# Performance work log

Hardware: AMD Instinct MI355X
Metric: run time of the kernel (lower is better)

Reference implementation:

```python
import jax, jax.numpy as jnp
import numpy as np
import math

NUM_PAGES = 256   # total KV pool pages
PAGE_SIZE = 16    # tokens per page
N_USED = 128      # pages in this sequence -> kv_len = 2048
H = 32            # num_heads
D = 128           # head_dim
LQ = 2048         # query length (== kv_len, causal prefill)


def setup_inputs() -> dict:
    key = jax.random.key(0)
    k_q, k_k, k_v, k_ks, k_vs = jax.random.split(key, 5)
    q = jax.random.normal(k_q, (1, H, LQ, D), dtype=jnp.float32)
    K_pages = jax.random.randint(k_k, (NUM_PAGES, PAGE_SIZE, H, D), -128, 128, dtype=jnp.int8)
    V_pages = jax.random.randint(k_v, (NUM_PAGES, PAGE_SIZE, H, D), -128, 128, dtype=jnp.int8)
    K_scale = jax.random.uniform(k_ks, (NUM_PAGES, 1, H, 1), dtype=jnp.float16, minval=0.001, maxval=0.02)
    V_scale = jax.random.uniform(k_vs, (NUM_PAGES, 1, H, 1), dtype=jnp.float16, minval=0.001, maxval=0.02)
    pages = jnp.arange(N_USED, dtype=jnp.int32)  # page table for this sequence
    return {"q": q, "K_pages": K_pages, "V_pages": V_pages,
            "K_scale": K_scale, "V_scale": V_scale, "pages": pages}


def _gather_dequant(pages_i8, scales, page_ids):
    # pages_i8: [P, ps, H, D] int8; scales: [P, 1, H, 1] fp16; page_ids: [n]
    x = pages_i8[page_ids].astype(jnp.float32) * scales[page_ids].astype(jnp.float32)
    n, ps, h, d = x.shape
    # cat along tokens, then [S,H,D] -> [1,H,S,D]
    return jnp.transpose(x.reshape(n * ps, h, d), (1, 0, 2))[None]


def reference(q, K_pages, V_pages, K_scale, V_scale, pages):
    K = _gather_dequant(K_pages, K_scale, pages)  # [1,H,S,D]
    V = _gather_dequant(V_pages, V_scale, pages)  # [1,H,S,D]
    lq = q.shape[2]
    s = K.shape[2]
    scale = 1.0 / math.sqrt(q.shape[-1])
    scores = jnp.einsum('bhqd,bhkd->bhqk', q, K) * scale  # [1,H,LQ,S]
    # torch is_causal: top-left aligned causal mask (j <= i)
    causal = jnp.tril(jnp.ones((lq, s), dtype=bool))
    scores = jnp.where(causal[None, None], scores, -jnp.inf)
    attn = jax.nn.softmax(scores, axis=-1)
    return jnp.einsum('bhqk,bhkd->bhqd', attn, V)
```

## Files before the change

### kernel.cpp

```cpp
#include <hip/hip_runtime.h>
#include <stdint.h>

#define NHEADS 32
#define DHEAD  128
#define LQ     2048
#define PAGE   16
#define QTILE  64
#define KVB    32
#define KPAD   136

typedef _Float16 f16x8 __attribute__((ext_vector_type(8)));
typedef float    f32x4 __attribute__((ext_vector_type(4)));

__global__ __launch_bounds__(256, 2)
void paged_attn_kernel(const float* __restrict__ q,
                       const int*   __restrict__ Kp,
                       const int*   __restrict__ Vp,
                       const float* __restrict__ Kscale,
                       const float* __restrict__ Vscale,
                       const int*   __restrict__ pages,
                       float* __restrict__ out)
{
    __shared__ _Float16 Ks[KVB][KPAD];
    __shared__ __align__(16) _Float16 Vt[DHEAD][KVB];
    __shared__ float    ksc[KVB];
    __shared__ _Float16 Ps[4][16][40];

    const int tid  = threadIdx.x;
    const int w    = tid >> 6;
    const int lane = tid & 63;
    const int g    = lane >> 4;
    const int c    = lane & 15;

    const int bx = blockIdx.x;
    const int h  = bx & (NHEADS - 1);
    const int nQT = gridDim.x >> 5;
    const int qt = nQT - 1 - (bx >> 5);
    const int q0 = qt * QTILE;

    const float qscale = 0.08838834764831845f * 1.44269504088896340736f;

    f16x8 qf[4];
    {
        const int qrow = q0 + w * 16 + c;
        const float* qp = q + ((size_t)h * LQ + qrow) * DHEAD;
        #pragma unroll
        for (int t = 0; t < 4; ++t) {
            const float* p = qp + t * 32 + g * 8;
            #pragma unroll
            for (int i = 0; i < 8; ++i)
                qf[t][i] = (_Float16)(p[i] * qscale);
        }
    }

    f32x4 o_acc[8];
    #pragma unroll
    for (int d = 0; d < 8; ++d) o_acc[d] = (f32x4){0.f, 0.f, 0.f, 0.f};
    float m_run[4], l_run[4];
    #pragma unroll
    for (int r = 0; r < 4; ++r) { m_run[r] = -1e30f; l_run[r] = 0.f; }

    const int ntiles = 2 * qt + 2;
    const int skv = tid >> 3;
    const int sa  = tid & 7;

    char* vtb = (char*)&Vt[0][0];

    auto issue = [&](int tile, int4* krD, int4* vrD, float& ksD, float& vsD) {
        const int t_glob = tile * KVB + skv;
        const int pg  = pages[t_glob >> 4];
        const int tok = t_glob & 15;
        const size_t base = (((size_t)pg * PAGE + tok) * NHEADS + h) * DHEAD + sa * 16;
        const int4* kp4 = (const int4*)(Kp + base);
        const int4* vp4 = (const int4*)(Vp + base);
        #pragma unroll
        for (int j = 0; j < 4; ++j) { krD[j] = kp4[j]; vrD[j] = vp4[j]; }
        vsD = Vscale[pg * NHEADS + h];
        if (tid < KVB) {
            const int pg2 = pages[(tile * KVB + tid) >> 4];
            ksD = Kscale[pg2 * NHEADS + h];
        }
    };

    int4 krA[4], vrA[4]; float kscA = 0.f, vsrA = 0.f;
    int4 krB[4], vrB[4]; float kscB = 0.f, vsrB = 0.f;
    issue(0, krA, vrA, kscA, vsrA);

    for (int tile = 0; tile < ntiles; ++tile) {
        const int kv0 = tile * KVB;

        {
            const int* ki = (const int*)krA;
            const int* vi = (const int*)vrA;
            f16x8 klo, khi;
            #pragma unroll
            for (int i = 0; i < 8; ++i) {
                klo[i] = (_Float16)ki[i];
                khi[i] = (_Float16)ki[8 + i];
            }
            *(f16x8*)&Ks[skv][sa * 16]     = klo;
            *(f16x8*)&Ks[skv][sa * 16 + 8] = khi;
            #pragma unroll
            for (int j = 0; j < 16; ++j) {
                const int dcol = sa * 16 + j;
                unsigned off = (unsigned)(dcol * (KVB * 2) + skv * 2);
                off ^= (unsigned)(((dcol >> 3) & 7) << 4);
                *(_Float16*)(vtb + off) = (_Float16)((float)vi[j] * vsrA);
            }
            if (tid < KVB) ksc[tid] = kscA;
        }
        __syncthreads();

        if (tile + 1 < ntiles) issue(tile + 1, krB, vrB, kscB, vsrB);

        const int q_wave_max = q0 + w * 16 + 15;
        if (kv0 <= q_wave_max) {
            f32x4 s[2];
            #pragma unroll
            for (int nt = 0; nt < 2; ++nt) {
                s[nt] = (f32x4){0.f, 0.f, 0.f, 0.f};
                #pragma unroll
                for (int t = 0; t < 4; ++t) {
                    f16x8 kf = *(const f16x8*)&Ks[nt * 16 + c][t * 32 + g * 8];
                    s[nt] = __builtin_amdgcn_mfma_f32_16x16x32_f16(qf[t], kf, s[nt], 0, 0, 0);
                }
            }
            const float ks0 = ksc[c],  ks1 = ksc[16 + c];
            const int kvg0 = kv0 + c, kvg1 = kv0 + 16 + c;
            const int qg   = q0 + w * 16 + g * 4;

            float tmax[4];
            #pragma unroll
            for (int r = 0; r < 4; ++r) {
                float s0 = s[0][r] * ks0;
                float s1 = s[1][r] * ks1;
                if (kvg0 > qg + r) s0 = -1e30f;
                if (kvg1 > qg + r) s1 = -1e30f;
                s[0][r] = s0; s[1][r] = s1;
                tmax[r] = fmaxf(s0, s1);
            }
            #pragma unroll
            for (int off = 1; off < 16; off <<= 1) {
                #pragma unroll
                for (int r = 0; r < 4; ++r)
                    tmax[r] = fmaxf(tmax[r], __shfl_xor(tmax[r], off, 64));
            }
            float alpha[4], rsum[4], p0[4], p1[4];
            #pragma unroll
            for (int r = 0; r < 4; ++r) {
                const float mn = fmaxf(m_run[r], tmax[r]);
                alpha[r] = exp2f(m_run[r] - mn);
                m_run[r] = mn;
                p0[r] = exp2f(s[0][r] - mn);
                p1[r] = exp2f(s[1][r] - mn);
                rsum[r] = p0[r] + p1[r];
            }
            #pragma unroll
            for (int off = 1; off < 16; off <<= 1) {
                #pragma unroll
                for (int r = 0; r < 4; ++r)
                    rsum[r] += __shfl_xor(rsum[r], off, 64);
            }
            #pragma unroll
            for (int r = 0; r < 4; ++r)
                l_run[r] = l_run[r] * alpha[r] + rsum[r];
            #pragma unroll
            for (int d = 0; d < 8; ++d)
                #pragma unroll
                for (int r = 0; r < 4; ++r)
                    o_acc[d][r] *= alpha[r];

            #pragma unroll
            for (int r = 0; r < 4; ++r) {
                Ps[w][g * 4 + r][c]      = (_Float16)p0[r];
                Ps[w][g * 4 + r][16 + c] = (_Float16)p1[r];
            }
            asm volatile("s_waitcnt lgkmcnt(0)" ::: "memory");
            f16x8 pf = *(const f16x8*)&Ps[w][c][g * 8];

            #pragma unroll
            for (int d = 0; d < 8; ++d) {
                const int dcol = d * 16 + c;
                unsigned off = (unsigned)(dcol * (KVB * 2) + g * 16);
                off ^= (unsigned)(((dcol >> 3) & 7) << 4);
                f16x8 vf = *(const f16x8*)(vtb + off);
                o_acc[d] = __builtin_amdgcn_mfma_f32_16x16x32_f16(pf, vf, o_acc[d], 0, 0, 0);
            }
        }
        __syncthreads();

        if (tile + 1 < ntiles) {
            #pragma unroll
            for (int j = 0; j < 4; ++j) { krA[j] = krB[j]; vrA[j] = vrB[j]; }
            kscA = kscB; vsrA = vsrB;
        }
    }

    const int qg = q0 + w * 16 + g * 4;
    float inv_l[4];
    #pragma unroll
    for (int r = 0; r < 4; ++r) inv_l[r] = 1.f / l_run[r];
    #pragma unroll
    for (int d = 0; d < 8; ++d) {
        #pragma unroll
        for (int r = 0; r < 4; ++r)
            out[((size_t)h * LQ + qg + r) * DHEAD + d * 16 + c] = o_acc[d][r] * inv_l[r];
    }
}

extern "C" void kernel_launch(void* const* d_in, const int* in_sizes, int n_in,
                              void* d_out, int out_size, void* d_ws, size_t ws_size,
                              hipStream_t stream) {
    (void)in_sizes; (void)n_in; (void)d_ws; (void)ws_size; (void)out_size;
    const float* qp = (const float*)d_in[0];
    const int*   kp = (const int*)d_in[1];
    const int*   vp = (const int*)d_in[2];
    const float* ks = (const float*)d_in[3];
    const float* vs = (const float*)d_in[4];
    const int*   pg = (const int*)d_in[5];
    float*       op = (float*)d_out;

    dim3 grid(NHEADS * (LQ / QTILE));
    dim3 block(256);
    paged_attn_kernel<<<grid, block, 0, stream>>>(qp, kp, vp, ks, vs, pg, op);
}
```

Measured before the change: 320.4 us.

## Pair complementary causal query tiles per block to balance work and reuse KV

Each block now handles two query tiles, p and NQT-1-p, for the same head, so every block does roughly the same amount of causal work. The dequantized K/V tiles staged in shared memory are shared by both query tiles, which halves KV loading and conversion per query. The grid shrinks from 1024 to 512 blocks. Each thread holds twice as many accumulators and Q fragments, which raises register pressure and may hurt occupancy under launch_bounds(256,2).

```diff
diff --git a/kernel.cpp b/kernel.cpp
--- a/kernel.cpp
+++ b/kernel.cpp
@@ -6,6 +6,7 @@
 #define LQ     2048
 #define PAGE   16
 #define QTILE  64
+#define NQT    32
 #define KVB    32
 #define KPAD   136
 
@@ -34,33 +35,34 @@
 
     const int bx = blockIdx.x;
     const int h  = bx & (NHEADS - 1);
-    const int nQT = gridDim.x >> 5;
-    const int qt = nQT - 1 - (bx >> 5);
-    const int q0 = qt * QTILE;
+    const int p  = bx >> 5;
+    const int qa = p, qb = NQT - 1 - p;
+    const int q0a = qa * QTILE, q0b = qb * QTILE;
 
     const float qscale = 0.08838834764831845f * 1.44269504088896340736f;
 
-    f16x8 qf[4];
+    f16x8 qfa[4], qfb[4];
     {
-        const int qrow = q0 + w * 16 + c;
-        const float* qp = q + ((size_t)h * LQ + qrow) * DHEAD;
+        const float* qpa = q + ((size_t)h * LQ + q0a + w * 16 + c) * DHEAD;
+        const float* qpb = q + ((size_t)h * LQ + q0b + w * 16 + c) * DHEAD;
         #pragma unroll
         for (int t = 0; t < 4; ++t) {
-            const float* p = qp + t * 32 + g * 8;
-            #pragma unroll
-            for (int i = 0; i < 8; ++i)
-                qf[t][i] = (_Float16)(p[i] * qscale);
+            #pragma unroll
+            for (int i = 0; i < 8; ++i) {
+                qfa[t][i] = (_Float16)(qpa[t * 32 + g * 8 + i] * qscale);
+                qfb[t][i] = (_Float16)(qpb[t * 32 + g * 8 + i] * qscale);
+            }
         }
     }
 
-    f32x4 o_acc[8];
-    #pragma unroll
-    for (int d = 0; d < 8; ++d) o_acc[d] = (f32x4){0.f, 0.f, 0.f, 0.f};
-    float m_run[4], l_run[4];
-    #pragma unroll
-    for (int r = 0; r < 4; ++r) { m_run[r] = -1e30f; l_run[r] = 0.f; }
-
-    const int ntiles = 2 * qt + 2;
+    f32x4 oaccA[8], oaccB[8];
+    float mA[4], lA[4], mB[4], lB[4];
+    #pragma unroll
+    for (int d = 0; d < 8; ++d) { oaccA[d] = (f32x4){0,0,0,0}; oaccB[d] = (f32x4){0,0,0,0}; }
+    #pragma unroll
+    for (int r = 0; r < 4; ++r) { mA[r] = mB[r] = -1e30f; lA[r] = lB[r] = 0.f; }
+
+    const int ntiles = 2 * qb + 2;
     const int skv = tid >> 3;
     const int sa  = tid & 7;
 
@@ -82,6 +84,79 @@
         }
     };
 
+    auto compute = [&](int kv0, const f16x8* qf, int q0t,
+                       f32x4* oacc, float* mr, float* lr) {
+        f32x4 s[2];
+        #pragma unroll
+        for (int nt = 0; nt < 2; ++nt) {
+            s[nt] = (f32x4){0,0,0,0};
+            #pragma unroll
+            for (int t = 0; t < 4; ++t) {
+                f16x8 kf = *(const f16x8*)&Ks[nt * 16 + c][t * 32 + g * 8];
+                s[nt] = __builtin_amdgcn_mfma_f32_16x16x32_f16(qf[t], kf, s[nt], 0, 0, 0);
+            }
+        }
+        const float ks0 = ksc[c],  ks1 = ksc[16 + c];
+        const int kvg0 = kv0 + c, kvg1 = kv0 + 16 + c;
+        const int qg   = q0t + w * 16 + g * 4;
+
+        float tmax[4];
+        #pragma unroll
+        for (int r = 0; r < 4; ++r) {
+            float s0 = s[0][r] * ks0;
+            float s1 = s[1][r] * ks1;
+            if (kvg0 > qg + r) s0 = -1e30f;
+            if (kvg1 > qg + r) s1 = -1e30f;
+            s[0][r] = s0; s[1][r] = s1;
+            tmax[r] = fmaxf(s0, s1);
+        }
+        #pragma unroll
+        for (int off = 1; off < 16; off <<= 1)
+            #pragma unroll
+            for (int r = 0; r < 4; ++r)
+                tmax[r] = fmaxf(tmax[r], __shfl_xor(tmax[r], off, 64));
+        float alpha[4], rsum[4], p0[4], p1[4];
+        #pragma unroll
+        for (int r = 0; r < 4; ++r) {
+            const float mn = fmaxf(mr[r], tmax[r]);
+            alpha[r] = exp2f(mr[r] - mn);
+            mr[r] = mn;
+            p0[r] = exp2f(s[0][r] - mn);
+            p1[r] = exp2f(s[1][r] - mn);
+            rsum[r] = p0[r] + p1[r];
+        }
+        #pragma unroll
+        for (int off = 1; off < 16; off <<= 1)
+            #pragma unroll
+            for (int r = 0; r < 4; ++r)
+                rsum[r] += __shfl_xor(rsum[r], off, 64);
+        #pragma unroll
+        for (int r = 0; r < 4; ++r)
+            lr[r] = lr[r] * alpha[r] + rsum[r];
+        #pragma unroll
+        for (int d = 0; d < 8; ++d)
+            #pragma unroll
+            for (int r = 0; r < 4; ++r)
+                oacc[d][r] *= alpha[r];
+
+        #pragma unroll
+        for (int r = 0; r < 4; ++r) {
+            Ps[w][g * 4 + r][c]      = (_Float16)p0[r];
+            Ps[w][g * 4 + r][16 + c] = (_Float16)p1[r];
+        }
+        asm volatile("s_waitcnt lgkmcnt(0)" ::: "memory");
+        f16x8 pf = *(const f16x8*)&Ps[w][c][g * 8];
+
+        #pragma unroll
+        for (int d = 0; d < 8; ++d) {
+            const int dcol = d * 16 + c;
+            unsigned off = (unsigned)(dcol * (KVB * 2) + g * 16);
+            off ^= (unsigned)(((dcol >> 3) & 7) << 4);
+            f16x8 vf = *(const f16x8*)(vtb + off);
+            oacc[d] = __builtin_amdgcn_mfma_f32_16x16x32_f16(pf, vf, oacc[d], 0, 0, 0);
+        }
+    };
+
     int4 krA[4], vrA[4]; float kscA = 0.f, vsrA = 0.f;
     int4 krB[4], vrB[4]; float kscB = 0.f, vsrB = 0.f;
     issue(0, krA, vrA, kscA, vsrA);
@@ -113,80 +188,11 @@
 
         if (tile + 1 < ntiles) issue(tile + 1, krB, vrB, kscB, vsrB);
 
-        const int q_wave_max = q0 + w * 16 + 15;
-        if (kv0 <= q_wave_max) {
-            f32x4 s[2];
-            #pragma unroll
-            for (int nt = 0; nt < 2; ++nt) {
-                s[nt] = (f32x4){0.f, 0.f, 0.f, 0.f};
-                #pragma unroll
-                for (int t = 0; t < 4; ++t) {
-                    f16x8 kf = *(const f16x8*)&Ks[nt * 16 + c][t * 32 + g * 8];
-                    s[nt] = __builtin_amdgcn_mfma_f32_16x16x32_f16(qf[t], kf, s[nt], 0, 0, 0);
-                }
-            }
-            const float ks0 = ksc[c],  ks1 = ksc[16 + c];
-            const int kvg0 = kv0 + c, kvg1 = kv0 + 16 + c;
-            const int qg   = q0 + w * 16 + g * 4;
-
-            float tmax[4];
-            #pragma unroll
-            for (int r = 0; r < 4; ++r) {
-                float s0 = s[0][r] * ks0;
-                float s1 = s[1][r] * ks1;
-                if (kvg0 > qg + r) s0 = -1e30f;
-                if (kvg1 > qg + r) s1 = -1e30f;
-                s[0][r] = s0; s[1][r] = s1;
-                tmax[r] = fmaxf(s0, s1);
-            }
-            #pragma unroll
-            for (int off = 1; off < 16; off <<= 1) {
-                #pragma unroll
-                for (int r = 0; r < 4; ++r)
-                    tmax[r] = fmaxf(tmax[r], __shfl_xor(tmax[r], off, 64));
-            }
-            float alpha[4], rsum[4], p0[4], p1[4];
-            #pragma unroll
-            for (int r = 0; r < 4; ++r) {
-                const float mn = fmaxf(m_run[r], tmax[r]);
-                alpha[r] = exp2f(m_run[r] - mn);
-                m_run[r] = mn;
-                p0[r] = exp2f(s[0][r] - mn);
-                p1[r] = exp2f(s[1][r] - mn);
-                rsum[r] = p0[r] + p1[r];
-            }
-            #pragma unroll
-            for (int off = 1; off < 16; off <<= 1) {
-                #pragma unroll
-                for (int r = 0; r < 4; ++r)
-                    rsum[r] += __shfl_xor(rsum[r], off, 64);
-            }
-            #pragma unroll
-            for (int r = 0; r < 4; ++r)
-                l_run[r] = l_run[r] * alpha[r] + rsum[r];
-            #pragma unroll
-            for (int d = 0; d < 8; ++d)
-                #pragma unroll
-                for (int r = 0; r < 4; ++r)
-                    o_acc[d][r] *= alpha[r];
-
-            #pragma unroll
-            for (int r = 0; r < 4; ++r) {
-                Ps[w][g * 4 + r][c]      = (_Float16)p0[r];
-                Ps[w][g * 4 + r][16 + c] = (_Float16)p1[r];
-            }
-            asm volatile("s_waitcnt lgkmcnt(0)" ::: "memory");
-            f16x8 pf = *(const f16x8*)&Ps[w][c][g * 8];
-
-            #pragma unroll
-            for (int d = 0; d < 8; ++d) {
-                const int dcol = d * 16 + c;
-                unsigned off = (unsigned)(dcol * (KVB * 2) + g * 16);
-                off ^= (unsigned)(((dcol >> 3) & 7) << 4);
-                f16x8 vf = *(const f16x8*)(vtb + off);
-                o_acc[d] = __builtin_amdgcn_mfma_f32_16x16x32_f16(pf, vf, o_acc[d], 0, 0, 0);
-            }
-        }
+        if (kv0 <= q0b + w * 16 + 15)
+            compute(kv0, qfb, q0b, oaccB, mB, lB);
+        if (kv0 <= q0a + w * 16 + 15)
+            compute(kv0, qfa, q0a, oaccA, mA, lA);
+
         __syncthreads();
 
         if (tile + 1 < ntiles) {
@@ -196,15 +202,17 @@
         }
     }
 
-    const int qg = q0 + w * 16 + g * 4;
-    float inv_l[4];
-    #pragma unroll
-    for (int r = 0; r < 4; ++r) inv_l[r] = 1.f / l_run[r];
+    #pragma unroll
+    for (int r = 0; r < 4; ++r) { lA[r] = 1.f / lA[r]; lB[r] = 1.f / lB[r]; }
+    const int qgA = q0a + w * 16 + g * 4;
+    const int qgB = q0b + w * 16 + g * 4;
     #pragma unroll
     for (int d = 0; d < 8; ++d) {
         #pragma unroll
-        for (int r = 0; r < 4; ++r)
-            out[((size_t)h * LQ + qg + r) * DHEAD + d * 16 + c] = o_acc[d][r] * inv_l[r];
+        for (int r = 0; r < 4; ++r) {
+            out[((size_t)h * LQ + qgA + r) * DHEAD + d * 16 + c] = oaccA[d][r] * lA[r];
+            out[((size_t)h * LQ + qgB + r) * DHEAD + d * 16 + c] = oaccB[d][r] * lB[r];
+        }
     }
 }
 
@@ -220,7 +228,7 @@
     const int*   pg = (const int*)d_in[5];
     float*       op = (float*)d_out;
 
-    dim3 grid(NHEADS * (LQ / QTILE));
+    dim3 grid(NHEADS * (NQT / 2));
     dim3 block(256);
     paged_attn_kernel<<<grid, block, 0, stream>>>(qp, kp, vp, ks, vs, pg, op);
 }
```

Result: no change. 315.8 us (-1.4%).
